# Kernel optimization log

Hardware: AMD Instinct MI355X
Metric: run time of the kernel (lower is better)

## Reference

```python
import jax, jax.numpy as jnp
import numpy as np

R = 4           # max_displacement
P = 2 * R + 1   # search_range = 9
DILATIONS = [[1], [1, 2, 3, 5, 9, 16]]
STRIDES = [4, 1]  # 8 // encoder_output_stride for strides [2, 8]
EPS = 1e-9


def _l2norm(x):
    # torch: x / (x.norm(dim=1, keepdim=True) + 1e-9)
    return x / (jnp.linalg.norm(x, axis=1, keepdims=True) + EPS)


def _corr(x1, x2, dilation, stride):
    """SpatialCorrelationSampler(patch_size=9, stride=stride, padding=0,
    dilation_patch=dilation): out[b,u,v,i,j] = sum_c x1[b,c,i*s,j*s] *
    x2[b,c,i*s+(u-R)*d, j*s+(v-R)*d], zero outside bounds."""
    B, C, H, W = x1.shape
    pad = R * dilation
    x2p = jnp.pad(x2, ((0, 0), (0, 0), (pad, pad), (pad, pad)))
    x1s = x1[:, :, ::stride, ::stride]  # (B,C,Ho,Wo)
    Ho, Wo = x1s.shape[2], x1s.shape[3]
    # all 81 (u,v) patch-offset slice starts in the padded map
    uv = jnp.stack(jnp.meshgrid(jnp.arange(P), jnp.arange(P), indexing='ij'),
                   axis=-1).reshape(-1, 2) * dilation  # (81, 2)

    def step(carry, start):
        x2uv = jax.lax.dynamic_slice(x2p, (0, 0, start[0], start[1]), (B, C, H, W))
        x2uv = x2uv[:, :, ::stride, ::stride]
        return carry, jnp.sum(x1s * x2uv, axis=1)  # (B,Ho,Wo)

    _, cost = jax.lax.scan(step, None, uv)  # (81,B,Ho,Wo)
    cost = cost.reshape(P, P, B, Ho, Wo)
    return jnp.transpose(cost, (2, 0, 1, 3, 4))  # (B,P,P,Ho,Wo)


def setup_inputs() -> dict:
    key = jax.random.key(0)
    k0, k1, k2, k3 = jax.random.split(key, 4)
    return {
        'x1_0': jax.random.normal(k0, (4, 256, 192, 256), dtype=jnp.float32),
        'x1_1': jax.random.normal(k1, (4, 256, 48, 64), dtype=jnp.float32),
        'x2_0': jax.random.normal(k2, (4, 256, 192, 256), dtype=jnp.float32),
        'x2_1': jax.random.normal(k3, (4, 256, 48, 64), dtype=jnp.float32),
    }


def reference(x1_0, x1_1, x2_0, x2_1):
    xs1, xs2 = [x1_0, x1_1], [x2_0, x2_1]
    cost_list = []
    for x1, x2, dils, s in zip(xs1, xs2, DILATIONS, STRIDES):
        x1n = _l2norm(x1)
        x2n = _l2norm(x2)
        per_dil = [_corr(x1n, x2n, d, s) for d in dils]  # each (B,P,P,Ho,Wo)
        # num_groups=1: per-dilation volumes stack into dim 1
        cost_list.append(jnp.stack(per_dil, axis=1))  # (B,nd,P,P,Ho,Wo)
    return jnp.concatenate(cost_list, axis=1)  # (B,7,9,9,48,64)
```

## Files before the change

kernel.cpp:

```cpp
#include <hip/hip_runtime.h>
#include <stdint.h>

#define EPSN 1e-9f

typedef __fp16 f16x8 __attribute__((ext_vector_type(8)));
typedef float f32x4 __attribute__((ext_vector_type(4)));

#define LDS_FENCE()                                        \
  do {                                                     \
    asm volatile("s_waitcnt lgkmcnt(0)" ::: "memory");     \
    __builtin_amdgcn_sched_barrier(0);                     \
  } while (0)


__global__ __launch_bounds__(256) void norms1_kernel(
    const float* __restrict__ x1_1, const float* __restrict__ x2_1,
    float* __restrict__ ws) {
  int p = blockIdx.x * 256 + threadIdx.x;
  const float* src = (p < 12288) ? x1_1 : x2_1;
  int q = (p < 12288) ? p : p - 12288;
  long base = (long)(q / 3072) * 786432 + (q % 3072);
  float ss = 0.f;
#pragma unroll 8
  for (int c = 0; c < 256; ++c) { float v = src[base + (long)c * 3072]; ss += v * v; }
  ws[p] = 1.f / (sqrtf(ss) + EPSN);
}

__global__ __launch_bounds__(256) void corr0_kernel(
    const float* __restrict__ x1, const float* __restrict__ x2,
    float* __restrict__ out) {
  int bx = blockIdx.x;
  int L = (bx & 7) * 96 + (bx >> 3);
  int y = L % 192, b = L / 192;
  int tid = threadIdx.x;
  int w = tid >> 6, lane = tid & 63;
  int i_lo = (y - 1) / 4; if (i_lo < 0) i_lo = 0;
  int i_hi = (y + 4) / 4; if (i_hi > 47) i_hi = 47;
  int NI = i_hi - i_lo + 1;

  __shared__ float red[4][34][64];
  __shared__ float inv2s[264];
  __shared__ float inv1s[3][64];

  float acc[3][9];
#pragma unroll
  for (int r = 0; r < 3; ++r)
#pragma unroll
    for (int v = 0; v < 9; ++v) acc[r][v] = 0.f;
  float sq0 = 0.f, sq1 = 0.f, sq2 = 0.f, sq3 = 0.f;
  float s1[3] = {0.f, 0.f, 0.f};

  const float* x2row = x2 + (long)b * 12582912 + (long)y * 256 + 4 * lane;
  const float* x1p[3];
#pragma unroll
  for (int r = 0; r < 3; ++r) {
    int ir = i_lo + r; if (ir > 47) ir = 47;
    x1p[r] = x1 + (long)b * 12582912 + (long)(4 * ir) * 256 + 4 * lane;
  }

#pragma unroll 4
  for (int cc = 0; cc < 64; ++cc) {
    long off = (long)(w * 64 + cc) * 49152;
    float4 f = *reinterpret_cast<const float4*>(x2row + off);
    sq0 += f.x * f.x; sq1 += f.y * f.y; sq2 += f.z * f.z; sq3 += f.w * f.w;
#pragma unroll
    for (int r = 0; r < 3; ++r) {
      float xv = x1p[r][off];
      float xr = __shfl_down(xv, 1);
      float xl = __shfl_up(xv, 1);
      s1[r] += xv * xv;
      acc[r][0] += xr * f.x; acc[r][1] += xr * f.y;
      acc[r][2] += xr * f.z; acc[r][3] += xr * f.w;
      acc[r][4] += xv * f.x; acc[r][5] += xv * f.y;
      acc[r][6] += xv * f.z; acc[r][7] += xv * f.w;
      acc[r][8] += xl * f.x;
    }
  }

#pragma unroll
  for (int r = 0; r < 3; ++r) {
    red[w][r * 9 + 0][lane] = __shfl_up(acc[r][0], 1);
    red[w][r * 9 + 1][lane] = __shfl_up(acc[r][1], 1);
    red[w][r * 9 + 2][lane] = __shfl_up(acc[r][2], 1);
    red[w][r * 9 + 3][lane] = __shfl_up(acc[r][3], 1);
    red[w][r * 9 + 4][lane] = acc[r][4];
    red[w][r * 9 + 5][lane] = acc[r][5];
    red[w][r * 9 + 6][lane] = acc[r][6];
    red[w][r * 9 + 7][lane] = acc[r][7];
    red[w][r * 9 + 8][lane] = __shfl_down(acc[r][8], 1);
    red[w][31 + r][lane] = s1[r];
  }
  red[w][27][lane] = sq0; red[w][28][lane] = sq1;
  red[w][29][lane] = sq2; red[w][30][lane] = sq3;
  __syncthreads();
  {
    int comp = tid & 3, jj = tid >> 2;
    float ss = red[0][27 + comp][jj] + red[1][27 + comp][jj] +
               red[2][27 + comp][jj] + red[3][27 + comp][jj];
    inv2s[4 + tid] = 1.f / (sqrtf(ss) + EPSN);
    if (tid < 4) { inv2s[tid] = 0.f; inv2s[260 + tid] = 0.f; }
    if (tid < 192) {
      int r = tid >> 6, j = tid & 63;
      float t = red[0][31 + r][j] + red[1][31 + r][j] +
                red[2][31 + r][j] + red[3][31 + r][j];
      inv1s[r][j] = 1.f / (sqrtf(t) + EPSN);
    }
  }
  __syncthreads();
  int lim = NI * 576;
  for (int idx = tid; idx < lim; idx += 256) {
    int r = idx / 576, rem = idx - r * 576;
    int v = rem >> 6, j = rem & 63;
    int i_r = i_lo + r;
    int u_r = y - 4 * i_r + 4;
    float s = red[0][r * 9 + v][j] + red[1][r * 9 + v][j] +
              red[2][r * 9 + v][j] + red[3][r * 9 + v][j];
    out[(long)b * 1741824 + (long)u_r * 27648 + (long)v * 3072 + i_r * 64 + j] =
        s * inv1s[r][j] * inv2s[4 * j + v];
  }
}

__global__ __launch_bounds__(256) void zfill0_kernel(float* __restrict__ out) {
  int idx = blockIdx.x * 256 + threadIdx.x;
  int b = idx / 2880, rem = idx - b * 2880;
  int k = rem / 576, rem2 = rem - k * 576;
  int v = rem2 >> 6, j = rem2 & 63;
  int u = (k < 4) ? k : 8;
  int i = (k < 4) ? 0 : 47;
  out[(long)b * 1741824 + (long)u * 27648 + (long)v * 3072 + i * 64 + j] = 0.f;
}

__global__ __launch_bounds__(256) void xpose1_kernel(
    const float* __restrict__ x1, const float* __restrict__ x2,
    __fp16* __restrict__ o1, __fp16* __restrict__ o2) {
  int bx = blockIdx.x;
  int tz = bx & 1; int rem = bx >> 1;
  int i = rem % 48, b = rem / 48;
  const float* src = tz ? x2 : x1;
  __fp16* dst = (tz ? o2 : o1) + (long)(b * 48 + i) * 16384;
  __shared__ uint32_t lds[64 * 128];
  __shared__ float sred[4][64];
  int t = threadIdx.x;
  int j = t & 63, cg = t >> 6;
  const float* sp = src + (long)b * 786432 + (long)i * 64 + j;
  float vv[64];
  float ss = 0.f;
#pragma unroll
  for (int c8 = 0; c8 < 64; ++c8) {
    float v = sp[(long)(cg * 64 + c8) * 3072];
    vv[c8] = v;
    ss += v * v;
  }
  sred[cg][j] = ss;
  __syncthreads();
  float invv = 1.f / (sqrtf(sred[0][j] + sred[1][j] + sred[2][j] + sred[3][j]) + EPSN);
#pragma unroll
  for (int cb = 0; cb < 8; ++cb) {
    uint32_t pk[4];
#pragma unroll
    for (int e2 = 0; e2 < 4; ++e2) {
      int cl = cb * 8 + e2 * 2;
      __fp16 h0 = (__fp16)(vv[cl] * invv);
      __fp16 h1 = (__fp16)(vv[cl + 1] * invv);
      pk[e2] = (uint32_t)__builtin_bit_cast(uint16_t, h0) |
               ((uint32_t)__builtin_bit_cast(uint16_t, h1) << 16);
    }
    int byteoff = j * 512 + ((cg * 128 + cb * 16) ^ ((j & 7) << 4));
    *reinterpret_cast<uint4*>(reinterpret_cast<char*>(lds) + byteoff) =
        make_uint4(pk[0], pk[1], pk[2], pk[3]);
  }
  __syncthreads();
#pragma unroll
  for (int rep = 0; rep < 8; ++rep) {
    int idx = rep * 256 + t;
    int jj = idx >> 5, cb = idx & 31;
    int byteoff = jj * 512 + ((cb * 16) ^ ((jj & 7) << 4));
    uint4 val = *reinterpret_cast<const uint4*>(
        reinterpret_cast<const char*>(lds) + byteoff);
    *reinterpret_cast<uint4*>(reinterpret_cast<char*>(dst) + jj * 512 + cb * 16) = val;
  }
}

__device__ const int OFFS39[39] = {
    0, 1, -1, 2, -2, 3, -3, 4, -4, 5, -5, 6, -6, 8, -8, 9, -9, 10, -10,
    12, -12, 15, -15, 16, -16, 18, -18, 20, -20, 27, -27, 32, -32, 36, -36,
    48, -48, 64, -64};

__global__ __launch_bounds__(64) void corr1m_kernel(
    const __fp16* __restrict__ w1, const __fp16* __restrict__ w2,
    float* __restrict__ out) {
  const int dils[6] = {1, 2, 3, 5, 9, 16};
  int bx = blockIdx.x;
  int L = (bx & 7) * 936 + (bx >> 3);
  int oi = L % 39, i = (L / 39) % 48, b = L / 1872;
  int o = OFFS39[oi];
  int y = i + o;
  bool valid = (y >= 0 && y < 48);
  int l = threadIdx.x;
  __shared__ float c_lds[64][65];

  if (valid) {
    int lm = l & 15, lk = l >> 4;
    const __fp16* A = w1 + (long)(b * 48 + i) * 16384;
    const __fp16* B = w2 + (long)(b * 48 + y) * 16384;
    f32x4 acc[4][4];
#pragma unroll
    for (int tm = 0; tm < 4; ++tm)
#pragma unroll
      for (int tn = 0; tn < 4; ++tn) acc[tm][tn] = (f32x4)0.f;

    for (int ks = 0; ks < 8; ++ks) {
      f16x8 af[4], bf[4];
      int ko = ks * 32 + lk * 8;
#pragma unroll
      for (int tm = 0; tm < 4; ++tm)
        af[tm] = __builtin_bit_cast(f16x8, *reinterpret_cast<const uint4*>(
                     A + (tm * 16 + lm) * 256 + ko));
#pragma unroll
      for (int tn = 0; tn < 4; ++tn)
        bf[tn] = __builtin_bit_cast(f16x8, *reinterpret_cast<const uint4*>(
                     B + (tn * 16 + lm) * 256 + ko));
#pragma unroll
      for (int tm = 0; tm < 4; ++tm)
#pragma unroll
        for (int tn = 0; tn < 4; ++tn)
          acc[tm][tn] = __builtin_amdgcn_mfma_f32_16x16x32_f16(
              af[tm], bf[tn], acc[tm][tn], 0, 0, 0);
    }
#pragma unroll
    for (int tm = 0; tm < 4; ++tm)
#pragma unroll
      for (int tn = 0; tn < 4; ++tn)
#pragma unroll
        for (int r = 0; r < 4; ++r)
          c_lds[tm * 16 + lk * 4 + r][tn * 16 + lm] = acc[tm][tn][r];
    LDS_FENCE();
  }

#pragma unroll
  for (int dI = 0; dI < 6; ++dI) {
    int d = dils[dI];
    if (o % d) continue;
    int ud = o / d;
    if (ud < -4 || ud > 4) continue;
    long ob = (long)b * 1741824 + (long)(1 + dI) * 248832 +
              (long)(ud + 4) * 27648 + (long)i * 64 + l;
#pragma unroll
    for (int v = 0; v < 9; ++v) {
      float val = 0.f;
      if (valid) {
        int j2 = l + (v - 4) * d;
        val = (j2 >= 0 && j2 < 64) ? c_lds[l][j2] : 0.f;
      }
      out[ob + (long)v * 3072] = val;
    }
  }
}

__global__ __launch_bounds__(64) void corr1_kernel(
    const float* __restrict__ x1, const float* __restrict__ x2,
    const float* __restrict__ ws, float* __restrict__ out) {
  int bx = blockIdx.x;
  int L = (bx & 7) * 1296 + (bx >> 3);
  int u = L % 9, dI = (L / 9) % 6, i = (L / 54) % 48, b = L / 2592;
  const int dils[6] = {1, 2, 3, 5, 9, 16};
  int d = dils[dI];
  int y = i + (u - 4) * d;
  int lane = threadIdx.x;
  long ob = (long)b * 1741824 + (long)(1 + dI) * 248832 + (long)u * 27648 +
            (long)i * 64 + lane;
  if (y < 0 || y >= 48) {
#pragma unroll
    for (int v = 0; v < 9; ++v) out[ob + v * 3072] = 0.f;
    return;
  }
  __shared__ uint4 x2t[192];
  x2t[lane] = make_uint4(0, 0, 0, 0);
  x2t[lane + 64] = make_uint4(0, 0, 0, 0);
  x2t[lane + 128] = make_uint4(0, 0, 0, 0);
  float acc[9];
#pragma unroll
  for (int v = 0; v < 9; ++v) acc[v] = 0.f;
  const float* x2row = x2 + (long)b * 786432 + (long)y * 64 + lane;
  const float* x1row = x1 + (long)b * 786432 + (long)i * 64 + lane;
#pragma unroll 1
  for (int cc8 = 0; cc8 < 32; ++cc8) {
    float x1v[8]; uint32_t xb[8];
#pragma unroll
    for (int cc = 0; cc < 8; ++cc) {
      long c = cc8 * 8 + cc;
      xb[cc] = __float_as_uint(x2row[c * 3072]) + 0x8000u;
      x1v[cc] = x1row[c * 3072];
    }
    uint4 pk;
    pk.x = (xb[0] >> 16) | (xb[1] & 0xffff0000u);
    pk.y = (xb[2] >> 16) | (xb[3] & 0xffff0000u);
    pk.z = (xb[4] >> 16) | (xb[5] & 0xffff0000u);
    pk.w = (xb[6] >> 16) | (xb[7] & 0xffff0000u);
    x2t[64 + lane] = pk;
    LDS_FENCE();
#pragma unroll
    for (int v = 0; v < 9; ++v) {
      uint4 q = x2t[64 + lane + (v - 4) * d];
      float s;
      s  = x1v[0] * __uint_as_float(q.x << 16);
      s += x1v[1] * __uint_as_float(q.x & 0xffff0000u);
      s += x1v[2] * __uint_as_float(q.y << 16);
      s += x1v[3] * __uint_as_float(q.y & 0xffff0000u);
      s += x1v[4] * __uint_as_float(q.z << 16);
      s += x1v[5] * __uint_as_float(q.z & 0xffff0000u);
      s += x1v[6] * __uint_as_float(q.w << 16);
      s += x1v[7] * __uint_as_float(q.w & 0xffff0000u);
      acc[v] += s;
    }
    LDS_FENCE();
  }
  const float* i1 = ws + b * 3072 + i * 64;
  const float* i2 = ws + 12288 + b * 3072 + y * 64;
  float inv1 = i1[lane];
#pragma unroll
  for (int v = 0; v < 9; ++v) {
    int col = lane + (v - 4) * d;
    float i2v = (col >= 0 && col < 64) ? i2[col] : 0.f;
    out[ob + v * 3072] = acc[v] * inv1 * i2v;
  }
}

extern "C" void kernel_launch(void* const* d_in, const int* in_sizes, int n_in,
                              void* d_out, int out_size, void* d_ws, size_t ws_size,
                              hipStream_t stream) {
  const float* x1_0 = (const float*)d_in[0];
  const float* x1_1 = (const float*)d_in[1];
  const float* x2_0 = (const float*)d_in[2];
  const float* x2_1 = (const float*)d_in[3];
  float* out = (float*)d_out;
  float* ws = (float*)d_ws;
  corr0_kernel<<<768, 256, 0, stream>>>(x1_0, x2_0, out);
  zfill0_kernel<<<45, 256, 0, stream>>>(out);
  if (ws_size >= 12681216) {
    __fp16* w1h = (__fp16*)((char*)d_ws + 98304);
    __fp16* w2h = w1h + 3145728;
    xpose1_kernel<<<384, 256, 0, stream>>>(x1_1, x2_1, w1h, w2h);
    corr1m_kernel<<<7488, 64, 0, stream>>>(w1h, w2h, out);
  } else {
    norms1_kernel<<<96, 256, 0, stream>>>(x1_1, x2_1, ws);
    corr1_kernel<<<10368, 64, 0, stream>>>(x1_1, x2_1, ws, out);
  }
}
```

Baseline: 122.4 us.

## Pre-normalize and transpose strided x1_0 into fp16 channel-contiguous buffer for corr0

Adds a pre-pass kernel that gathers the stride-4 samples of x1_0, L2-normalizes them and stores them as fp16 with channels contiguous per pixel, using an XOR-swizzled LDS transpose. The main correlation kernel then reads eight channels per 16-byte load for the centre, left and right neighbours, instead of strided scalar fp32 loads plus cross-lane shuffles. It also drops the per-block x1 norm reduction. In exchange there is an extra kernel launch, a workspace dependency and lower precision for x1. The old kernel is kept as a fallback when the workspace is too small.

```diff
diff --git a/kernel.cpp b/kernel.cpp
--- a/kernel.cpp
+++ b/kernel.cpp
@@ -26,8 +26,56 @@
   ws[p] = 1.f / (sqrtf(ss) + EPSN);
 }
 
-__global__ __launch_bounds__(256) void corr0_kernel(
-    const float* __restrict__ x1, const float* __restrict__ x2,
+__global__ __launch_bounds__(256) void xpose0_kernel(
+    const float* __restrict__ x1, __fp16* __restrict__ x1h0) {
+  int bx = blockIdx.x;
+  int i = bx % 48, b = bx / 48;
+  __fp16* dst = x1h0 + (long)(b * 48 + i) * 16384;
+  __shared__ uint32_t lds[64 * 128];
+  __shared__ float sred[4][64];
+  int t = threadIdx.x;
+  int j = t & 63, cg = t >> 6;
+  const float* sp = x1 + (long)b * 12582912 + (long)(4 * i) * 256 + 4 * j;
+  float vv[64];
+  float ss = 0.f;
+#pragma unroll
+  for (int c8 = 0; c8 < 64; ++c8) {
+    float v = sp[(long)(cg * 64 + c8) * 49152];
+    vv[c8] = v;
+    ss += v * v;
+  }
+  sred[cg][j] = ss;
+  __syncthreads();
+  float invv = 1.f / (sqrtf(sred[0][j] + sred[1][j] + sred[2][j] + sred[3][j]) + EPSN);
+#pragma unroll
+  for (int cb = 0; cb < 8; ++cb) {
+    uint32_t pk[4];
+#pragma unroll
+    for (int e2 = 0; e2 < 4; ++e2) {
+      int cl = cb * 8 + e2 * 2;
+      __fp16 h0 = (__fp16)(vv[cl] * invv);
+      __fp16 h1 = (__fp16)(vv[cl + 1] * invv);
+      pk[e2] = (uint32_t)__builtin_bit_cast(uint16_t, h0) |
+               ((uint32_t)__builtin_bit_cast(uint16_t, h1) << 16);
+    }
+    int byteoff = j * 512 + ((cg * 128 + cb * 16) ^ ((j & 7) << 4));
+    *reinterpret_cast<uint4*>(reinterpret_cast<char*>(lds) + byteoff) =
+        make_uint4(pk[0], pk[1], pk[2], pk[3]);
+  }
+  __syncthreads();
+#pragma unroll
+  for (int rep = 0; rep < 8; ++rep) {
+    int idx = rep * 256 + t;
+    int jj = idx >> 5, cb = idx & 31;
+    int byteoff = jj * 512 + ((cb * 16) ^ ((jj & 7) << 4));
+    uint4 val = *reinterpret_cast<const uint4*>(
+        reinterpret_cast<const char*>(lds) + byteoff);
+    *reinterpret_cast<uint4*>(reinterpret_cast<char*>(dst) + jj * 512 + cb * 16) = val;
+  }
+}
+
+__global__ __launch_bounds__(256) void corr0f_kernel(
+    const __fp16* __restrict__ x1h, const float* __restrict__ x2,
     float* __restrict__ out) {
   int bx = blockIdx.x;
   int L = (bx & 7) * 96 + (bx >> 3);
@@ -38,10 +86,112 @@
   int i_hi = (y + 4) / 4; if (i_hi > 47) i_hi = 47;
   int NI = i_hi - i_lo + 1;
 
+  __shared__ float red[4][31][64];
+  __shared__ float inv2s[264];
+
+  float acc[3][9];
+#pragma unroll
+  for (int r = 0; r < 3; ++r)
+#pragma unroll
+    for (int v = 0; v < 9; ++v) acc[r][v] = 0.f;
+  float sq0 = 0.f, sq1 = 0.f, sq2 = 0.f, sq3 = 0.f;
+
+  const float* x2row = x2 + (long)b * 12582912 + (long)y * 256 + 4 * lane;
+  int lm = (lane == 0) ? 0 : lane - 1;
+  int lp = (lane == 63) ? 63 : lane + 1;
+  const __fp16 *pc[3], *pl[3], *pr[3];
+#pragma unroll
+  for (int r = 0; r < 3; ++r) {
+    int ir = i_lo + r; if (ir > 47) ir = 47;
+    const __fp16* base = x1h + (long)(b * 48 + ir) * 16384;
+    pc[r] = base + lane * 256;
+    pl[r] = base + lm * 256;
+    pr[r] = base + lp * 256;
+  }
+
+#pragma unroll 1
+  for (int g = 0; g < 8; ++g) {
+    int c0 = w * 64 + g * 8;
+    float4 fv[8];
+#pragma unroll
+    for (int e = 0; e < 8; ++e)
+      fv[e] = *reinterpret_cast<const float4*>(x2row + (long)(c0 + e) * 49152);
+    f16x8 hc[3], hl[3], hr[3];
+#pragma unroll
+    for (int r = 0; r < 3; ++r) {
+      hc[r] = __builtin_bit_cast(f16x8, *reinterpret_cast<const uint4*>(pc[r] + c0));
+      hl[r] = __builtin_bit_cast(f16x8, *reinterpret_cast<const uint4*>(pl[r] + c0));
+      hr[r] = __builtin_bit_cast(f16x8, *reinterpret_cast<const uint4*>(pr[r] + c0));
+    }
+#pragma unroll
+    for (int e = 0; e < 8; ++e) {
+      float4 f = fv[e];
+      sq0 += f.x * f.x; sq1 += f.y * f.y; sq2 += f.z * f.z; sq3 += f.w * f.w;
+#pragma unroll
+      for (int r = 0; r < 3; ++r) {
+        float xv  = (float)hc[r][e];
+        float xrr = (float)hr[r][e];
+        float xll = (float)hl[r][e];
+        acc[r][0] += xrr * f.x; acc[r][1] += xrr * f.y;
+        acc[r][2] += xrr * f.z; acc[r][3] += xrr * f.w;
+        acc[r][4] += xv * f.x;  acc[r][5] += xv * f.y;
+        acc[r][6] += xv * f.z;  acc[r][7] += xv * f.w;
+        acc[r][8] += xll * f.x;
+      }
+    }
+  }
+
+#pragma unroll
+  for (int r = 0; r < 3; ++r) {
+    acc[r][0] = __shfl_up(acc[r][0], 1);
+    acc[r][1] = __shfl_up(acc[r][1], 1);
+    acc[r][2] = __shfl_up(acc[r][2], 1);
+    acc[r][3] = __shfl_up(acc[r][3], 1);
+    acc[r][8] = __shfl_down(acc[r][8], 1);
+  }
+
+#pragma unroll
+  for (int r = 0; r < 3; ++r)
+#pragma unroll
+    for (int v = 0; v < 9; ++v) red[w][r * 9 + v][lane] = acc[r][v];
+  red[w][27][lane] = sq0; red[w][28][lane] = sq1;
+  red[w][29][lane] = sq2; red[w][30][lane] = sq3;
+  __syncthreads();
+  {
+    int comp = tid & 3, jj = tid >> 2;
+    float ss = red[0][27 + comp][jj] + red[1][27 + comp][jj] +
+               red[2][27 + comp][jj] + red[3][27 + comp][jj];
+    inv2s[4 + tid] = 1.f / (sqrtf(ss) + EPSN);
+    if (tid < 4) { inv2s[tid] = 0.f; inv2s[260 + tid] = 0.f; }
+  }
+  __syncthreads();
+  int lim = NI * 576;
+  for (int idx = tid; idx < lim; idx += 256) {
+    int r = idx / 576, rem = idx - r * 576;
+    int v = rem >> 6, j = rem & 63;
+    int i_r = i_lo + r;
+    int u_r = y - 4 * i_r + 4;
+    float s = red[0][r * 9 + v][j] + red[1][r * 9 + v][j] +
+              red[2][r * 9 + v][j] + red[3][r * 9 + v][j];
+    out[(long)b * 1741824 + (long)u_r * 27648 + (long)v * 3072 + i_r * 64 + j] =
+        s * inv2s[4 * j + v];
+  }
+}
+
+__global__ __launch_bounds__(256) void corr0_fb_kernel(
+    const float* __restrict__ x1b, const float* __restrict__ x2,
+    float* __restrict__ out) {
+  int bx = blockIdx.x;
+  int L = (bx & 7) * 96 + (bx >> 3);
+  int y = L % 192, b = L / 192;
+  int tid = threadIdx.x;
+  int w = tid >> 6, lane = tid & 63;
+  int i_lo = (y - 1) / 4; if (i_lo < 0) i_lo = 0;
+  int i_hi = (y + 4) / 4; if (i_hi > 47) i_hi = 47;
+  int NI = i_hi - i_lo + 1;
   __shared__ float red[4][34][64];
   __shared__ float inv2s[264];
   __shared__ float inv1s[3][64];
-
   float acc[3][9];
 #pragma unroll
   for (int r = 0; r < 3; ++r)
@@ -49,23 +199,23 @@
     for (int v = 0; v < 9; ++v) acc[r][v] = 0.f;
   float sq0 = 0.f, sq1 = 0.f, sq2 = 0.f, sq3 = 0.f;
   float s1[3] = {0.f, 0.f, 0.f};
-
   const float* x2row = x2 + (long)b * 12582912 + (long)y * 256 + 4 * lane;
   const float* x1p[3];
 #pragma unroll
   for (int r = 0; r < 3; ++r) {
     int ir = i_lo + r; if (ir > 47) ir = 47;
-    x1p[r] = x1 + (long)b * 12582912 + (long)(4 * ir) * 256 + 4 * lane;
-  }
-
+    x1p[r] = x1b + (long)b * 12582912 + (long)ir * 1024 + (long)lane * 4;
+  }
 #pragma unroll 4
   for (int cc = 0; cc < 64; ++cc) {
-    long off = (long)(w * 64 + cc) * 49152;
-    float4 f = *reinterpret_cast<const float4*>(x2row + off);
+    int c = w * 64 + cc;
+    long off2 = (long)c * 49152;
+    long off1 = (long)c * 49152;
+    float4 f = *reinterpret_cast<const float4*>(x2row + off2);
     sq0 += f.x * f.x; sq1 += f.y * f.y; sq2 += f.z * f.z; sq3 += f.w * f.w;
 #pragma unroll
     for (int r = 0; r < 3; ++r) {
-      float xv = x1p[r][off];
+      float xv = x1p[r][off1];
       float xr = __shfl_down(xv, 1);
       float xl = __shfl_up(xv, 1);
       s1[r] += xv * xv;
@@ -76,7 +226,6 @@
       acc[r][8] += xl * f.x;
     }
   }
-
 #pragma unroll
   for (int r = 0; r < 3; ++r) {
     red[w][r * 9 + 0][lane] = __shfl_up(acc[r][0], 1);
@@ -335,7 +484,13 @@
   const float* x2_1 = (const float*)d_in[3];
   float* out = (float*)d_out;
   float* ws = (float*)d_ws;
-  corr0_kernel<<<768, 256, 0, stream>>>(x1_0, x2_0, out);
+  if (ws_size >= 18972672) {
+    __fp16* x1h0 = (__fp16*)((char*)d_ws + 12681216);
+    xpose0_kernel<<<192, 256, 0, stream>>>(x1_0, x1h0);
+    corr0f_kernel<<<768, 256, 0, stream>>>(x1h0, x2_0, out);
+  } else {
+    corr0_fb_kernel<<<768, 256, 0, stream>>>(x1_0, x2_0, out);
+  }
   zfill0_kernel<<<45, 256, 0, stream>>>(out);
   if (ws_size >= 12681216) {
     __fp16* w1h = (__fp16*)((char*)d_ws + 98304);
```

New measurement: 138.0 us. +12.7%, slower.
